# Kernel optimization log

Measured on AMD Instinct MI355X. Metric: run time of the kernel, lower is better.

Reference implementation:

```python
import jax, jax.numpy as jnp
import numpy as np

BATCH, DIM, K = 32768, 512, 512


def setup_inputs() -> dict:
    key = jax.random.key(0)
    k1, k2 = jax.random.split(key)
    x = jax.random.normal(k1, (BATCH, DIM), dtype=jnp.float32)
    means = jax.random.normal(k2, (K, DIM), dtype=jnp.float32) / jnp.sqrt(jnp.float32(DIM))
    log_vars = jnp.zeros((K, 1), dtype=jnp.float32)
    log_weights = jnp.zeros((K,), dtype=jnp.float32)
    return {"x": x, "means": means, "log_vars": log_vars, "log_weights": log_weights}


def reference(x, means, log_vars, log_weights):
    # spherical covariance path of DifferentiableGMM.forward
    dim = x.shape[1]
    inv_vars = jnp.exp(-log_vars[:, 0])  # (K,) 1/var_k
    x_sq = jnp.sum(x * x, axis=1, keepdims=True)            # (B,1)
    mu_sq = jnp.sum(means * means, axis=1)                   # (K,)
    cross = x @ means.T                                      # (B,K) GEMM
    sq_dist = x_sq - 2.0 * cross + mu_sq[None, :]            # (B,K)
    sq_mahal = sq_dist * inv_vars[None, :]                   # (B,K)
    log_det = dim * log_vars[:, 0]                           # (K,)
    log_lik = -0.5 * (sq_mahal + log_det[None, :])           # (B,K)
    log_post = log_lik + jax.nn.log_softmax(log_weights)[None, :]
    return jax.nn.softmax(log_post, axis=1)                  # responsibilities (B,K)
```

## Files before the change

### kernel.cpp

```cpp
#include <hip/hip_runtime.h>
#include <stdint.h>

#define BATCH 32768
#define DIM   512
#define KCLS  512

typedef __bf16    bf16x8 __attribute__((ext_vector_type(8)));
typedef float     f32x4  __attribute__((ext_vector_type(4)));
typedef uint16_t  u16x4  __attribute__((ext_vector_type(4)));
typedef uint16_t  u16x8  __attribute__((ext_vector_type(8)));

__device__ __forceinline__ uint16_t f2bf(float f) {
    uint32_t u = __float_as_uint(f);
    u += 0x7FFFu + ((u >> 16) & 1u);
    return (uint16_t)(u >> 16);
}

__global__ __launch_bounds__(64) void gmm_prep(
    const float* __restrict__ means,
    const float* __restrict__ log_vars,
    const float* __restrict__ log_weights,
    uint16_t* __restrict__ Bsw,
    float* __restrict__ invv_a,
    float* __restrict__ alpha_a,
    float* __restrict__ beta_a)
{
    const int k = blockIdx.x;
    const int l = threadIdx.x;

    const float* mrow = means + (size_t)k * DIM + l * 8;
    f32x4 v0 = *(const f32x4*)(mrow);
    f32x4 v1 = *(const f32x4*)(mrow + 4);

    u16x8 pk;
    pk[0] = f2bf(v0[0]); pk[1] = f2bf(v0[1]); pk[2] = f2bf(v0[2]); pk[3] = f2bf(v0[3]);
    pk[4] = f2bf(v1[0]); pk[5] = f2bf(v1[1]); pk[6] = f2bf(v1[2]); pk[7] = f2bf(v1[3]);

    const int c16 = k >> 4, r = k & 15, ch = l >> 2, hh = l & 3;
    *(u16x8*)(Bsw + ((((c16 * 16) + ch) * 64) + (hh * 16 + r)) * 8) = pk;

    float sq = v0[0]*v0[0] + v0[1]*v0[1] + v0[2]*v0[2] + v0[3]*v0[3]
             + v1[0]*v1[0] + v1[1]*v1[1] + v1[2]*v1[2] + v1[3]*v1[3];
    #pragma unroll
    for (int m = 1; m <= 32; m <<= 1) sq += __shfl_xor(sq, m);

    if (l == 0) {
        const float lv = log_vars[k];
        const float iv = __expf(-lv);
        invv_a[k]  = iv;
        alpha_a[k] = -0.5f * iv;
        beta_a[k]  = -0.5f * (sq * iv + (float)DIM * lv) + log_weights[k];
    }
}

__global__ __launch_bounds__(256, 2) void gmm_main(
    const float* __restrict__ x,
    const uint16_t* __restrict__ Bsw,
    const float* __restrict__ invv_a,
    const float* __restrict__ alpha_a,
    const float* __restrict__ beta_a,
    float* __restrict__ out)
{
    __shared__ uint16_t As[32][72];
    __shared__ float xsq_lds[32];
    __shared__ float pmax[4][32];
    __shared__ float psum[4][32];

    const int t    = threadIdx.x;
    const int w    = t >> 6;
    const int lane = t & 63;
    const int r16  = lane & 15;
    const int h    = lane >> 4;
    const int row0 = blockIdx.x * 32;

    const int srow = t >> 3;
    const int sp   = t & 7;

    f32x4 acc[2][8];
    #pragma unroll
    for (int rt = 0; rt < 2; ++rt)
        #pragma unroll
        for (int ct = 0; ct < 8; ++ct)
            acc[rt][ct] = (f32x4){0.f, 0.f, 0.f, 0.f};

    float xsq_priv = 0.f;
    const float* xrow = x + (size_t)(row0 + srow) * DIM + sp * 4;
    const uint16_t* bbase = Bsw + (size_t)w * 65536 + (size_t)lane * 8;

    f32x4 a_pref = *(const f32x4*)xrow;

    for (int chk = 0; chk < 16; ++chk) {
        f32x4 av = a_pref;
        if (chk < 15) a_pref = *(const f32x4*)(xrow + (chk + 1) * 32);

        xsq_priv += av[0]*av[0] + av[1]*av[1] + av[2]*av[2] + av[3]*av[3];
        u16x4 pk;
        pk[0] = f2bf(av[0]); pk[1] = f2bf(av[1]);
        pk[2] = f2bf(av[2]); pk[3] = f2bf(av[3]);

        __syncthreads();
        *(u16x4*)&As[srow][sp * 4] = pk;
        __syncthreads();

        bf16x8 afrag0 = *(const bf16x8*)&As[r16][8 * h];
        bf16x8 afrag1 = *(const bf16x8*)&As[16 + r16][8 * h];

        bf16x8 bfrag[8];
        #pragma unroll
        for (int ct = 0; ct < 8; ++ct)
            bfrag[ct] = *(const bf16x8*)(bbase + ct * 8192 + chk * 512);

        #pragma unroll
        for (int ct = 0; ct < 8; ++ct) {
            acc[0][ct] = __builtin_amdgcn_mfma_f32_16x16x32_bf16(afrag0, bfrag[ct], acc[0][ct], 0, 0, 0);
            acc[1][ct] = __builtin_amdgcn_mfma_f32_16x16x32_bf16(afrag1, bfrag[ct], acc[1][ct], 0, 0, 0);
        }
    }

    xsq_priv += __shfl_xor(xsq_priv, 1);
    xsq_priv += __shfl_xor(xsq_priv, 2);
    xsq_priv += __shfl_xor(xsq_priv, 4);
    if (sp == 0) xsq_lds[srow] = xsq_priv;
    __syncthreads();

    float invv[8], alf[8], bet[8];
    #pragma unroll
    for (int ct = 0; ct < 8; ++ct) {
        const int col = 128 * w + 16 * ct + r16;
        invv[ct] = invv_a[col];
        alf[ct]  = alpha_a[col];
        bet[ct]  = beta_a[col];
    }
    float xsq[2][4];
    #pragma unroll
    for (int rt = 0; rt < 2; ++rt)
        #pragma unroll
        for (int reg = 0; reg < 4; ++reg)
            xsq[rt][reg] = xsq_lds[16 * rt + 4 * h + reg];

    float mr[2][4];
    #pragma unroll
    for (int rt = 0; rt < 2; ++rt) {
        #pragma unroll
        for (int reg = 0; reg < 4; ++reg) {
            float m = -1e30f;
            #pragma unroll
            for (int ct = 0; ct < 8; ++ct) {
                const float v = acc[rt][ct][reg] * invv[ct] + (alf[ct] * xsq[rt][reg] + bet[ct]);
                acc[rt][ct][reg] = v;
                m = fmaxf(m, v);
            }
            m = fmaxf(m, __shfl_xor(m, 1));
            m = fmaxf(m, __shfl_xor(m, 2));
            m = fmaxf(m, __shfl_xor(m, 4));
            m = fmaxf(m, __shfl_xor(m, 8));
            mr[rt][reg] = m;
        }
    }
    if (r16 == 0) {
        #pragma unroll
        for (int rt = 0; rt < 2; ++rt)
            #pragma unroll
            for (int reg = 0; reg < 4; ++reg)
                pmax[w][16 * rt + 4 * h + reg] = mr[rt][reg];
    }
    __syncthreads();

    float sr[2][4];
    #pragma unroll
    for (int rt = 0; rt < 2; ++rt) {
        #pragma unroll
        for (int reg = 0; reg < 4; ++reg) {
            const int rl = 16 * rt + 4 * h + reg;
            const float m = fmaxf(fmaxf(pmax[0][rl], pmax[1][rl]),
                                  fmaxf(pmax[2][rl], pmax[3][rl]));
            float s = 0.f;
            #pragma unroll
            for (int ct = 0; ct < 8; ++ct) {
                const float e = __expf(acc[rt][ct][reg] - m);
                acc[rt][ct][reg] = e;
                s += e;
            }
            s += __shfl_xor(s, 1);
            s += __shfl_xor(s, 2);
            s += __shfl_xor(s, 4);
            s += __shfl_xor(s, 8);
            sr[rt][reg] = s;
        }
    }
    if (r16 == 0) {
        #pragma unroll
        for (int rt = 0; rt < 2; ++rt)
            #pragma unroll
            for (int reg = 0; reg < 4; ++reg)
                psum[w][16 * rt + 4 * h + reg] = sr[rt][reg];
    }
    __syncthreads();

    #pragma unroll
    for (int rt = 0; rt < 2; ++rt) {
        #pragma unroll
        for (int reg = 0; reg < 4; ++reg) {
            const int rl = 16 * rt + 4 * h + reg;
            const float tot = (psum[0][rl] + psum[1][rl]) + (psum[2][rl] + psum[3][rl]);
            const float rinv = 1.0f / tot;
            float* orow = out + (size_t)(row0 + rl) * KCLS + 128 * w + r16;
            #pragma unroll
            for (int ct = 0; ct < 8; ++ct)
                orow[16 * ct] = acc[rt][ct][reg] * rinv;
        }
    }
}

extern "C" void kernel_launch(void* const* d_in, const int* in_sizes, int n_in,
                              void* d_out, int out_size, void* d_ws, size_t ws_size,
                              hipStream_t stream) {
    (void)in_sizes; (void)n_in; (void)out_size; (void)ws_size;
    const float* x           = (const float*)d_in[0];
    const float* means       = (const float*)d_in[1];
    const float* log_vars    = (const float*)d_in[2];
    const float* log_weights = (const float*)d_in[3];
    float* out = (float*)d_out;

    uint16_t* Bsw = (uint16_t*)d_ws;
    float* invv_a  = (float*)((char*)d_ws + (512u << 10));
    float* alpha_a = invv_a + KCLS;
    float* beta_a  = alpha_a + KCLS;

    gmm_prep<<<KCLS, 64, 0, stream>>>(means, log_vars, log_weights,
                                      Bsw, invv_a, alpha_a, beta_a);
    gmm_main<<<BATCH / 32, 256, 0, stream>>>(x, Bsw, invv_a, alpha_a, beta_a, out);
}
```

Baseline: 159.6 us.

## Load A fragments directly from global, drop LDS staging and barriers

Each wave now loads its own x rows straight from global memory into MFMA A-fragment registers, converting to bf16 in registers. This removes the shared-memory staging buffer and the two __syncthreads per k-chunk. The cost is that all four waves redundantly load the same 32 rows of x, which quadruples L1/L2 read traffic for x. Occupancy is raised to three blocks per SIMD, and the prep kernel packs four classes per block.

```diff
diff --git a/kernel.cpp b/kernel.cpp
--- a/kernel.cpp
+++ b/kernel.cpp
@@ -7,7 +7,7 @@
 
 typedef __bf16    bf16x8 __attribute__((ext_vector_type(8)));
 typedef float     f32x4  __attribute__((ext_vector_type(4)));
-typedef uint16_t  u16x4  __attribute__((ext_vector_type(4)));
+typedef float     f32x8  __attribute__((ext_vector_type(8)));
 typedef uint16_t  u16x8  __attribute__((ext_vector_type(8)));
 
 __device__ __forceinline__ uint16_t f2bf(float f) {
@@ -16,7 +16,9 @@
     return (uint16_t)(u >> 16);
 }
 
-__global__ __launch_bounds__(64) void gmm_prep(
+union bfcast { u16x8 u; bf16x8 b; };
+
+__global__ __launch_bounds__(256) void gmm_prep(
     const float* __restrict__ means,
     const float* __restrict__ log_vars,
     const float* __restrict__ log_weights,
@@ -25,8 +27,8 @@
     float* __restrict__ alpha_a,
     float* __restrict__ beta_a)
 {
-    const int k = blockIdx.x;
-    const int l = threadIdx.x;
+    const int k = blockIdx.x * 4 + (threadIdx.x >> 6);
+    const int l = threadIdx.x & 63;
 
     const float* mrow = means + (size_t)k * DIM + l * 8;
     f32x4 v0 = *(const f32x4*)(mrow);
@@ -53,7 +55,7 @@
     }
 }
 
-__global__ __launch_bounds__(256, 2) void gmm_main(
+__global__ __launch_bounds__(256, 3) void gmm_main(
     const float* __restrict__ x,
     const uint16_t* __restrict__ Bsw,
     const float* __restrict__ invv_a,
@@ -61,8 +63,6 @@
     const float* __restrict__ beta_a,
     float* __restrict__ out)
 {
-    __shared__ uint16_t As[32][72];
-    __shared__ float xsq_lds[32];
     __shared__ float pmax[4][32];
     __shared__ float psum[4][32];
 
@@ -73,9 +73,6 @@
     const int h    = lane >> 4;
     const int row0 = blockIdx.x * 32;
 
-    const int srow = t >> 3;
-    const int sp   = t & 7;
-
     f32x4 acc[2][8];
     #pragma unroll
     for (int rt = 0; rt < 2; ++rt)
@@ -83,27 +80,24 @@
         for (int ct = 0; ct < 8; ++ct)
             acc[rt][ct] = (f32x4){0.f, 0.f, 0.f, 0.f};
 
-    float xsq_priv = 0.f;
-    const float* xrow = x + (size_t)(row0 + srow) * DIM + sp * 4;
+    const float* xA = x + (size_t)(row0 + r16) * DIM + 8 * h;
     const uint16_t* bbase = Bsw + (size_t)w * 65536 + (size_t)lane * 8;
 
-    f32x4 a_pref = *(const f32x4*)xrow;
+    float xsq0 = 0.f, xsq1 = 0.f;
 
     for (int chk = 0; chk < 16; ++chk) {
-        f32x4 av = a_pref;
-        if (chk < 15) a_pref = *(const f32x4*)(xrow + (chk + 1) * 32);
-
-        xsq_priv += av[0]*av[0] + av[1]*av[1] + av[2]*av[2] + av[3]*av[3];
-        u16x4 pk;
-        pk[0] = f2bf(av[0]); pk[1] = f2bf(av[1]);
-        pk[2] = f2bf(av[2]); pk[3] = f2bf(av[3]);
-
-        __syncthreads();
-        *(u16x4*)&As[srow][sp * 4] = pk;
-        __syncthreads();
-
-        bf16x8 afrag0 = *(const bf16x8*)&As[r16][8 * h];
-        bf16x8 afrag1 = *(const bf16x8*)&As[16 + r16][8 * h];
+        const float* pa = xA + 32 * chk;
+        f32x8 a0 = *(const f32x8*)(pa);
+        f32x8 a1 = *(const f32x8*)(pa + 16 * DIM);
+
+        bfcast c0, c1;
+        #pragma unroll
+        for (int j = 0; j < 8; ++j) {
+            xsq0 += a0[j] * a0[j];
+            xsq1 += a1[j] * a1[j];
+            c0.u[j] = f2bf(a0[j]);
+            c1.u[j] = f2bf(a1[j]);
+        }
 
         bf16x8 bfrag[8];
         #pragma unroll
@@ -112,16 +106,19 @@
 
         #pragma unroll
         for (int ct = 0; ct < 8; ++ct) {
-            acc[0][ct] = __builtin_amdgcn_mfma_f32_16x16x32_bf16(afrag0, bfrag[ct], acc[0][ct], 0, 0, 0);
-            acc[1][ct] = __builtin_amdgcn_mfma_f32_16x16x32_bf16(afrag1, bfrag[ct], acc[1][ct], 0, 0, 0);
-        }
-    }
-
-    xsq_priv += __shfl_xor(xsq_priv, 1);
-    xsq_priv += __shfl_xor(xsq_priv, 2);
-    xsq_priv += __shfl_xor(xsq_priv, 4);
-    if (sp == 0) xsq_lds[srow] = xsq_priv;
-    __syncthreads();
+            acc[0][ct] = __builtin_amdgcn_mfma_f32_16x16x32_bf16(c0.b, bfrag[ct], acc[0][ct], 0, 0, 0);
+            acc[1][ct] = __builtin_amdgcn_mfma_f32_16x16x32_bf16(c1.b, bfrag[ct], acc[1][ct], 0, 0, 0);
+        }
+    }
+
+    xsq0 += __shfl_xor(xsq0, 16); xsq0 += __shfl_xor(xsq0, 32);
+    xsq1 += __shfl_xor(xsq1, 16); xsq1 += __shfl_xor(xsq1, 32);
+    float xsq[2][4];
+    #pragma unroll
+    for (int reg = 0; reg < 4; ++reg) {
+        xsq[0][reg] = __shfl(xsq0, 4 * h + reg);
+        xsq[1][reg] = __shfl(xsq1, 4 * h + reg);
+    }
 
     float invv[8], alf[8], bet[8];
     #pragma unroll
@@ -131,12 +128,6 @@
         alf[ct]  = alpha_a[col];
         bet[ct]  = beta_a[col];
     }
-    float xsq[2][4];
-    #pragma unroll
-    for (int rt = 0; rt < 2; ++rt)
-        #pragma unroll
-        for (int reg = 0; reg < 4; ++reg)
-            xsq[rt][reg] = xsq_lds[16 * rt + 4 * h + reg];
 
     float mr[2][4];
     #pragma unroll
@@ -227,7 +218,7 @@
     float* alpha_a = invv_a + KCLS;
     float* beta_a  = alpha_a + KCLS;
 
-    gmm_prep<<<KCLS, 64, 0, stream>>>(means, log_vars, log_weights,
-                                      Bsw, invv_a, alpha_a, beta_a);
+    gmm_prep<<<KCLS / 4, 256, 0, stream>>>(means, log_vars, log_weights,
+                                           Bsw, invv_a, alpha_a, beta_a);
     gmm_main<<<BATCH / 32, 256, 0, stream>>>(x, Bsw, invv_a, alpha_a, beta_a, out);
 }
```

Measured after the change: 169.9 us. 1.06x slower.
